# Optimization experiments

Measured on AMD Instinct MI355X. Metric: run time of the kernel, lower is better.

The kernel has to match this reference:

```python
import jax, jax.numpy as jnp
import numpy as np

NFIELD, NKER = 8, 16
B, Y, X, P, T = 32, 32, 32, 16, 8


def setup_inputs() -> dict:
    key = jax.random.key(0)
    k1, k2 = jax.random.split(key)
    fieldpatch = jax.random.normal(k1, (B, NFIELD, Y, X, P, T), dtype=jnp.float32)
    quadpatch = jax.random.uniform(k2, (B, Y, X, P, T), dtype=jnp.float32)
    zeros_fk = jnp.zeros((NFIELD, NKER), dtype=jnp.float32)
    return {
        "fieldpatch": fieldpatch,
        "quadpatch": quadpatch,
        "mean_lat": zeros_fk, "logstd_lat": zeros_fk,
        "mean_lon": zeros_fk, "logstd_lon": zeros_fk,
        "mean_lev": zeros_fk, "logstd_lev": zeros_fk,
        "logtau_time": zeros_fk,
    }


def _gaussian1d(mean, logstd, length):
    # (f, k, length): exp(-0.5*((coord - mean)/std)^2), coord in [-1, 1]
    coord = jnp.linspace(-1.0, 1.0, length, dtype=mean.dtype)
    std = jnp.exp(logstd)
    z = (coord[None, None, :] - mean[..., None]) / std[..., None]
    return jnp.exp(-0.5 * z * z)


def _exponential1d(logtau, length):
    # (f, k, length): exp(-coord / tau), coord = 0..length-1
    coord = jnp.arange(length, dtype=logtau.dtype)
    tau = jnp.exp(logtau) + 1e-4
    return jnp.exp(-coord[None, None, :] / tau[..., None])


def reference(fieldpatch, quadpatch, mean_lat, logstd_lat, mean_lon, logstd_lon,
              mean_lev, logstd_lev, logtau_time):
    b, f, y, x, p, t = fieldpatch.shape
    ky = _gaussian1d(mean_lat, logstd_lat, y)      # (f,k,y)
    kx = _gaussian1d(mean_lon, logstd_lon, x)      # (f,k,x)
    kp = _gaussian1d(mean_lev, logstd_lev, p)      # (f,k,p)
    kt = _exponential1d(logtau_time, t)            # (f,k,t)
    # Separable outer product -> full kernel (f,k,y,x,p,t)
    kernel = jnp.einsum('fky,fkx,fkp,fkt->fkyxpt', ky, kx, kp, kt)
    qmean = quadpatch.mean(axis=0)                 # (y,x,p,t)
    integral = jnp.einsum('fkyxpt,yxpt->fk', kernel, qmean) + 1e-4
    weights = kernel / integral[:, :, None, None, None, None]
    # torch weights() runs under @torch.no_grad(): weights are constant wrt autograd
    weights = jax.lax.stop_gradient(weights)
    features = jnp.einsum('bfyxpt,fkyxpt,byxpt->bfk', fieldpatch, weights, quadpatch)
    return features.reshape(b, -1)
```

## Files before the change

### kernel.cpp

```cpp
#include <hip/hip_runtime.h>
#include <math.h>

#define NF 8
#define NK 16
#define BB 32
#define YY 32
#define XX 32
#define PP 16
#define TT 8
#define YX (YY*XX)
#define PT (PP*TT)
#define YXPT (YX*PT)
#define CHUNKS 8
#define COLS_PER_BLOCK (YX/CHUNKS)
#define COLS_PER_WAVE  (COLS_PER_BLOCK/4)
#define MAIN_ITERS     (COLS_PER_WAVE/2)
#define STEP           ((2*PT)/4)

#define QMEAN_OFF 0
#define ACC_OFF   (QMEAN_OFF + YXPT)
#define INTG_OFF  (ACC_OFF + CHUNKS*BB*NF*NK)

__global__ __launch_bounds__(256) void k_qmean(const float* __restrict__ quad,
                                               float* __restrict__ ws) {
    const int tid = threadIdx.x, bx = blockIdx.x;
    __shared__ float4 sm[256];
    const int j4 = bx * 32 + (tid & 31);
    const int bg = tid >> 5;
    const float4* q4 = (const float4*)quad;
    float4 a = make_float4(0.f, 0.f, 0.f, 0.f);
    #pragma unroll
    for (int i = 0; i < 4; ++i) {
        float4 v = q4[(size_t)(bg * 4 + i) * (YXPT / 4) + j4];
        a.x += v.x; a.y += v.y; a.z += v.z; a.w += v.w;
    }
    sm[tid] = a;
    __syncthreads();
    if (tid < 32) {
        float4 r = sm[tid];
        #pragma unroll
        for (int g = 1; g < 8; ++g) {
            float4 v = sm[tid + 32 * g];
            r.x += v.x; r.y += v.y; r.z += v.z; r.w += v.w;
        }
        r.x *= (1.f / BB); r.y *= (1.f / BB); r.z *= (1.f / BB); r.w *= (1.f / BB);
        ((float4*)(ws + QMEAN_OFF))[j4] = r;
    }
}

__global__ __launch_bounds__(256) void k_integral(
    const float* __restrict__ mean_lat, const float* __restrict__ logstd_lat,
    const float* __restrict__ mean_lon, const float* __restrict__ logstd_lon,
    const float* __restrict__ mean_lev, const float* __restrict__ logstd_lev,
    const float* __restrict__ logtau, float* __restrict__ ws) {
    const int fk = blockIdx.x >> 2, qr = blockIdx.x & 3;
    const int tid = threadIdx.x;
    const float mlat = mean_lat[fk], islat = expf(-logstd_lat[fk]);
    const float mlon = mean_lon[fk], islon = expf(-logstd_lon[fk]);
    const float mlev = mean_lev[fk], islev = expf(-logstd_lev[fk]);
    const float itau = 1.f / (expf(logtau[fk]) + 1e-4f);

    __shared__ __align__(16) float wpt[PT];
    if (tid < PT) {
        const float cp = -1.f + 2.f * (float)(tid >> 3) / (PP - 1);
        const float zp = (cp - mlev) * islev;
        wpt[tid] = expf(-0.5f * zp * zp - (float)(tid & 7) * itau);
    }
    __syncthreads();

    const int yx = qr * 256 + tid;
    const float cy = -1.f + 2.f * (float)(yx >> 5) / (YY - 1);
    const float cx = -1.f + 2.f * (float)(yx & 31) / (XX - 1);
    const float zy = (cy - mlat) * islat;
    const float zx = (cx - mlon) * islon;
    const float wyx = expf(-0.5f * (zy * zy + zx * zx));

    const float4* q4 = (const float4*)(ws + QMEAN_OFF + (size_t)yx * PT);
    const float4* w4 = (const float4*)wpt;
    float s = 0.f;
    #pragma unroll
    for (int j = 0; j < PT / 4; ++j) {
        float4 w = w4[j], q = q4[j];
        s += w.x * q.x + w.y * q.y + w.z * q.z + w.w * q.w;
    }
    float partial = wyx * s;
    #pragma unroll
    for (int m = 32; m; m >>= 1) partial += __shfl_xor(partial, m);
    __shared__ float red[4];
    if ((tid & 63) == 0) red[tid >> 6] = partial;
    __syncthreads();
    if (tid == 0)
        ws[INTG_OFF + qr * (NF * NK) + fk] = red[0] + red[1] + red[2] + red[3];
}


#define KQ(WC, K) do {                                                          \
    float poly = fmaf(ga.w, r[K], ga.z);                                        \
    poly = fmaf(poly, r[K], ga.y);                                              \
    poly = fmaf(poly, r[K], ga.x);                                              \
    acc[K] = fmaf(WC, poly, acc[K]);                                            \
} while (0)

#define COLPAIR_COMPUTE(WVP) do {                                               \
    float4 ga;                                                                  \
    ga.x = fa.x*qa.x; ga.y = fa.y*qa.y; ga.z = fa.z*qa.z; ga.w = fa.w*qa.w;     \
    float4 w0 = (WVP)[0], w1 = (WVP)[1], w2 = (WVP)[2], w3 = (WVP)[3];          \
    KQ(w0.x, 0);  KQ(w0.y, 1);  KQ(w0.z, 2);  KQ(w0.w, 3);                      \
    KQ(w1.x, 4);  KQ(w1.y, 5);  KQ(w1.z, 6);  KQ(w1.w, 7);                      \
    KQ(w2.x, 8);  KQ(w2.y, 9);  KQ(w2.z, 10); KQ(w2.w, 11);                     \
    KQ(w3.x, 12); KQ(w3.y, 13); KQ(w3.z, 14); KQ(w3.w, 15);                     \
} while (0)

__global__ __launch_bounds__(256) void k_main(
    const float* __restrict__ field, const float* __restrict__ quad,
    const float* __restrict__ mean_lat, const float* __restrict__ logstd_lat,
    const float* __restrict__ mean_lon, const float* __restrict__ logstd_lon,
    const float* __restrict__ mean_lev, const float* __restrict__ logstd_lev,
    const float* __restrict__ logtau, float* __restrict__ ws)
{
    const int bx = blockIdx.x;
    const int qg2 = bx >> 6, f = (bx >> 3) & 7, rr0 = bx & 7;
    const int bc = qg2 * 8 + rr0;
    const int b = bc >> 3, chunk = bc & 7;
    const int tid = threadIdx.x;
    const int wave = tid >> 6, L = tid & 63;
    const int half = L >> 5, qg = L & 31;

    const int colBase = chunk * COLS_PER_BLOCK + wave * COLS_PER_WAVE;
    const float4* fp = (const float4*)(field + (size_t)(b * NF + f) * YXPT + (size_t)colBase * PT) + L;
    const float4* qp = (const float4*)(quad  + (size_t)b * YXPT            + (size_t)colBase * PT) + L;

    float4 fbuf[4], qbuf[4];
    #pragma unroll
    for (int j = 0; j < 4; ++j) { fbuf[j] = fp[j * STEP]; qbuf[j] = qp[j * STEP]; }

    __shared__ __align__(16) float sw[COLS_PER_BLOCK * NK];
    __shared__ float wptab[NK * PP];
    __shared__ float prm[NK][8];

    if (tid < NK) {
        const int fk = f * NK + tid;
        prm[tid][0] = mean_lat[fk];
        prm[tid][1] = expf(-logstd_lat[fk]);
        prm[tid][2] = mean_lon[fk];
        prm[tid][3] = expf(-logstd_lon[fk]);
        prm[tid][4] = mean_lev[fk];
        prm[tid][5] = expf(-logstd_lev[fk]);
        const float itau = 1.f / (expf(logtau[fk]) + 1e-4f);
        const float rk = expf(-itau);
        prm[tid][6] = rk;
        prm[tid][7] = rk * rk * rk * rk;
    }
    __syncthreads();

    #pragma unroll
    for (int i = 0; i < 8; ++i) {
        const int e = i * 256 + tid;
        const int col = e >> 4, k = e & 15;
        const int yx = chunk * COLS_PER_BLOCK + col;
        const float cy = -1.f + 2.f * (float)(yx >> 5) / (YY - 1);
        const float cx = -1.f + 2.f * (float)(yx & 31) / (XX - 1);
        const float zy = (cy - prm[k][0]) * prm[k][1];
        const float zx = (cx - prm[k][2]) * prm[k][3];
        sw[col * NK + k] = expf(-0.5f * (zy * zy + zx * zx));
    }
    {
        const int k = tid >> 4, p = tid & 15;
        const float cp = -1.f + 2.f * (float)p / (PP - 1);
        const float zp = (cp - prm[k][4]) * prm[k][5];
        wptab[tid] = expf(-0.5f * zp * zp);
    }
    __syncthreads();

    float r[NK];
    #pragma unroll
    for (int k = 0; k < NK; ++k)
        r[k] = __int_as_float(__builtin_amdgcn_readfirstlane(__float_as_int(prm[k][6])));

    float acc[NK];
    #pragma unroll
    for (int k = 0; k < NK; ++k) acc[k] = 0.f;

    const float* swp = sw + (wave * COLS_PER_WAVE + half) * NK;

    #pragma unroll 1
    for (int so = 0; so < 3; ++so) {
        fp += 4 * STEP; qp += 4 * STEP;
        #pragma unroll
        for (int j = 0; j < 4; ++j) {
            float4 fa = fbuf[j], qa = qbuf[j];
            fbuf[j] = fp[j * STEP]; qbuf[j] = qp[j * STEP];
            const float4* wvp = (const float4*)(swp + j * (2 * NK));
            COLPAIR_COMPUTE(wvp);
        }
        swp += 4 * (2 * NK);
    }
    #pragma unroll
    for (int j = 0; j < 4; ++j) {
        float4 fa = fbuf[j], qa = qbuf[j];
        const float4* wvp = (const float4*)(swp + j * (2 * NK));
        COLPAIR_COMPUTE(wvp);
    }

    {
        const int p = qg >> 1, hi = qg & 1;
        #pragma unroll
        for (int k = 0; k < NK; ++k) {
            const float wp = wptab[k * PP + p];
            const float ck = hi ? wp * prm[k][7] : wp;
            acc[k] *= ck;
        }
    }

    __shared__ float red[4][NK];
    #pragma unroll
    for (int k = 0; k < NK; ++k) {
        float v = acc[k];
        v += __shfl_xor(v, 32); v += __shfl_xor(v, 16); v += __shfl_xor(v, 8);
        v += __shfl_xor(v, 4);  v += __shfl_xor(v, 2);  v += __shfl_xor(v, 1);
        if (L == 0) red[wave][k] = v;
    }
    __syncthreads();
    if (tid < NK) {
        float s2 = red[0][tid] + red[1][tid] + red[2][tid] + red[3][tid];
        ws[ACC_OFF + chunk * (BB * NF * NK) + (b * NF + f) * NK + tid] = s2;
    }
}

__global__ void k_final(const float* __restrict__ ws, float* __restrict__ out) {
    int i = blockIdx.x * 256 + threadIdx.x;
    if (i >= BB * NF * NK) return;
    float a = 0.f;
    #pragma unroll
    for (int c = 0; c < CHUNKS; ++c) a += ws[ACC_OFF + c * (BB * NF * NK) + i];
    const int fk = i & (NF * NK - 1);
    float g = 1e-4f;
    #pragma unroll
    for (int q = 0; q < 4; ++q) g += ws[INTG_OFF + q * (NF * NK) + fk];
    out[i] = a / g;
}

extern "C" void kernel_launch(void* const* d_in, const int* in_sizes, int n_in,
                              void* d_out, int out_size, void* d_ws, size_t ws_size,
                              hipStream_t stream) {
    const float* field = (const float*)d_in[0];
    const float* quad  = (const float*)d_in[1];
    float* ws = (float*)d_ws;

    k_qmean<<<1024, 256, 0, stream>>>(quad, ws);
    k_integral<<<NF * NK * 4, 256, 0, stream>>>(
        (const float*)d_in[2], (const float*)d_in[3],
        (const float*)d_in[4], (const float*)d_in[5],
        (const float*)d_in[6], (const float*)d_in[7],
        (const float*)d_in[8], ws);
    k_main<<<BB * NF * CHUNKS, 256, 0, stream>>>(field, quad,
        (const float*)d_in[2], (const float*)d_in[3],
        (const float*)d_in[4], (const float*)d_in[5],
        (const float*)d_in[6], (const float*)d_in[7],
        (const float*)d_in[8], ws);
    k_final<<<(BB * NF * NK + 255) / 256, 256, 0, stream>>>(ws, (float*)d_out);
}
```

Baseline: 232.4 us.

## Merge qmean and main kernels into one launch, deepen prefetch to eight column pairs

The qmean reduction and the main feature-accumulation kernel become one launch. The first 1024 blocks compute the batch mean of quadpatch and the remaining blocks do the main work, so the two can run concurrently and one launch boundary is removed. The integral kernel moves after the fused kernel, which it needs since it reads the qmean. The main loop now prefetches all eight column pairs of a half at once instead of four per iteration, which raises memory-level parallelism at the cost of more registers.

```diff
diff --git a/kernel.cpp b/kernel.cpp
--- a/kernel.cpp
+++ b/kernel.cpp
@@ -14,84 +14,12 @@
 #define CHUNKS 8
 #define COLS_PER_BLOCK (YX/CHUNKS)
 #define COLS_PER_WAVE  (COLS_PER_BLOCK/4)
-#define MAIN_ITERS     (COLS_PER_WAVE/2)
 #define STEP           ((2*PT)/4)
+#define QMEAN_BLOCKS   1024
 
 #define QMEAN_OFF 0
 #define ACC_OFF   (QMEAN_OFF + YXPT)
 #define INTG_OFF  (ACC_OFF + CHUNKS*BB*NF*NK)
-
-__global__ __launch_bounds__(256) void k_qmean(const float* __restrict__ quad,
-                                               float* __restrict__ ws) {
-    const int tid = threadIdx.x, bx = blockIdx.x;
-    __shared__ float4 sm[256];
-    const int j4 = bx * 32 + (tid & 31);
-    const int bg = tid >> 5;
-    const float4* q4 = (const float4*)quad;
-    float4 a = make_float4(0.f, 0.f, 0.f, 0.f);
-    #pragma unroll
-    for (int i = 0; i < 4; ++i) {
-        float4 v = q4[(size_t)(bg * 4 + i) * (YXPT / 4) + j4];
-        a.x += v.x; a.y += v.y; a.z += v.z; a.w += v.w;
-    }
-    sm[tid] = a;
-    __syncthreads();
-    if (tid < 32) {
-        float4 r = sm[tid];
-        #pragma unroll
-        for (int g = 1; g < 8; ++g) {
-            float4 v = sm[tid + 32 * g];
-            r.x += v.x; r.y += v.y; r.z += v.z; r.w += v.w;
-        }
-        r.x *= (1.f / BB); r.y *= (1.f / BB); r.z *= (1.f / BB); r.w *= (1.f / BB);
-        ((float4*)(ws + QMEAN_OFF))[j4] = r;
-    }
-}
-
-__global__ __launch_bounds__(256) void k_integral(
-    const float* __restrict__ mean_lat, const float* __restrict__ logstd_lat,
-    const float* __restrict__ mean_lon, const float* __restrict__ logstd_lon,
-    const float* __restrict__ mean_lev, const float* __restrict__ logstd_lev,
-    const float* __restrict__ logtau, float* __restrict__ ws) {
-    const int fk = blockIdx.x >> 2, qr = blockIdx.x & 3;
-    const int tid = threadIdx.x;
-    const float mlat = mean_lat[fk], islat = expf(-logstd_lat[fk]);
-    const float mlon = mean_lon[fk], islon = expf(-logstd_lon[fk]);
-    const float mlev = mean_lev[fk], islev = expf(-logstd_lev[fk]);
-    const float itau = 1.f / (expf(logtau[fk]) + 1e-4f);
-
-    __shared__ __align__(16) float wpt[PT];
-    if (tid < PT) {
-        const float cp = -1.f + 2.f * (float)(tid >> 3) / (PP - 1);
-        const float zp = (cp - mlev) * islev;
-        wpt[tid] = expf(-0.5f * zp * zp - (float)(tid & 7) * itau);
-    }
-    __syncthreads();
-
-    const int yx = qr * 256 + tid;
-    const float cy = -1.f + 2.f * (float)(yx >> 5) / (YY - 1);
-    const float cx = -1.f + 2.f * (float)(yx & 31) / (XX - 1);
-    const float zy = (cy - mlat) * islat;
-    const float zx = (cx - mlon) * islon;
-    const float wyx = expf(-0.5f * (zy * zy + zx * zx));
-
-    const float4* q4 = (const float4*)(ws + QMEAN_OFF + (size_t)yx * PT);
-    const float4* w4 = (const float4*)wpt;
-    float s = 0.f;
-    #pragma unroll
-    for (int j = 0; j < PT / 4; ++j) {
-        float4 w = w4[j], q = q4[j];
-        s += w.x * q.x + w.y * q.y + w.z * q.z + w.w * q.w;
-    }
-    float partial = wyx * s;
-    #pragma unroll
-    for (int m = 32; m; m >>= 1) partial += __shfl_xor(partial, m);
-    __shared__ float red[4];
-    if ((tid & 63) == 0) red[tid >> 6] = partial;
-    __syncthreads();
-    if (tid == 0)
-        ws[INTG_OFF + qr * (NF * NK) + fk] = red[0] + red[1] + red[2] + red[3];
-}
 
 
 #define KQ(WC, K) do {                                                          \
@@ -111,18 +39,49 @@
     KQ(w3.x, 12); KQ(w3.y, 13); KQ(w3.z, 14); KQ(w3.w, 15);                     \
 } while (0)
 
-__global__ __launch_bounds__(256) void k_main(
+__global__ __launch_bounds__(256) void k_fused(
     const float* __restrict__ field, const float* __restrict__ quad,
     const float* __restrict__ mean_lat, const float* __restrict__ logstd_lat,
     const float* __restrict__ mean_lon, const float* __restrict__ logstd_lon,
     const float* __restrict__ mean_lev, const float* __restrict__ logstd_lev,
     const float* __restrict__ logtau, float* __restrict__ ws)
 {
-    const int bx = blockIdx.x;
+    const int tid = threadIdx.x;
+    const int bx0 = blockIdx.x;
+    __shared__ __align__(16) float smem[2432];
+    __shared__ float red[4][NK];
+
+    if (bx0 < QMEAN_BLOCKS) {
+        float4* sm = (float4*)smem;
+        const int j4 = bx0 * 32 + (tid & 31);
+        const int bg = tid >> 5;
+        const float4* q4 = (const float4*)quad;
+        float4 a = make_float4(0.f, 0.f, 0.f, 0.f);
+        #pragma unroll
+        for (int i = 0; i < 4; ++i) {
+            float4 v = q4[(size_t)(bg * 4 + i) * (YXPT / 4) + j4];
+            a.x += v.x; a.y += v.y; a.z += v.z; a.w += v.w;
+        }
+        sm[tid] = a;
+        __syncthreads();
+        if (tid < 32) {
+            float4 rr = sm[tid];
+            #pragma unroll
+            for (int g = 1; g < 8; ++g) {
+                float4 v = sm[tid + 32 * g];
+                rr.x += v.x; rr.y += v.y; rr.z += v.z; rr.w += v.w;
+            }
+            rr.x *= (1.f / BB); rr.y *= (1.f / BB);
+            rr.z *= (1.f / BB); rr.w *= (1.f / BB);
+            ((float4*)(ws + QMEAN_OFF))[j4] = rr;
+        }
+        return;
+    }
+
+    const int bx = bx0 - QMEAN_BLOCKS;
     const int qg2 = bx >> 6, f = (bx >> 3) & 7, rr0 = bx & 7;
     const int bc = qg2 * 8 + rr0;
     const int b = bc >> 3, chunk = bc & 7;
-    const int tid = threadIdx.x;
     const int wave = tid >> 6, L = tid & 63;
     const int half = L >> 5, qg = L & 31;
 
@@ -130,13 +89,13 @@
     const float4* fp = (const float4*)(field + (size_t)(b * NF + f) * YXPT + (size_t)colBase * PT) + L;
     const float4* qp = (const float4*)(quad  + (size_t)b * YXPT            + (size_t)colBase * PT) + L;
 
-    float4 fbuf[4], qbuf[4];
-    #pragma unroll
-    for (int j = 0; j < 4; ++j) { fbuf[j] = fp[j * STEP]; qbuf[j] = qp[j * STEP]; }
-
-    __shared__ __align__(16) float sw[COLS_PER_BLOCK * NK];
-    __shared__ float wptab[NK * PP];
-    __shared__ float prm[NK][8];
+    float4 fbuf[8], qbuf[8];
+    #pragma unroll
+    for (int j = 0; j < 8; ++j) { fbuf[j] = fp[j * STEP]; qbuf[j] = qp[j * STEP]; }
+
+    float* sw = smem;
+    float* wptab = smem + 2048;
+    float (*prm)[8] = (float (*)[8])(smem + 2304);
 
     if (tid < NK) {
         const int fk = f * NK + tid;
@@ -183,22 +142,21 @@
 
     const float* swp = sw + (wave * COLS_PER_WAVE + half) * NK;
 
-    #pragma unroll 1
-    for (int so = 0; so < 3; ++so) {
-        fp += 4 * STEP; qp += 4 * STEP;
+    {
+        const float4* fp2 = fp + 8 * STEP;
+        const float4* qp2 = qp + 8 * STEP;
         #pragma unroll
-        for (int j = 0; j < 4; ++j) {
+        for (int j = 0; j < 8; ++j) {
             float4 fa = fbuf[j], qa = qbuf[j];
-            fbuf[j] = fp[j * STEP]; qbuf[j] = qp[j * STEP];
+            fbuf[j] = fp2[j * STEP]; qbuf[j] = qp2[j * STEP];
             const float4* wvp = (const float4*)(swp + j * (2 * NK));
             COLPAIR_COMPUTE(wvp);
         }
-        swp += 4 * (2 * NK);
-    }
-    #pragma unroll
-    for (int j = 0; j < 4; ++j) {
+    }
+    #pragma unroll
+    for (int j = 0; j < 8; ++j) {
         float4 fa = fbuf[j], qa = qbuf[j];
-        const float4* wvp = (const float4*)(swp + j * (2 * NK));
+        const float4* wvp = (const float4*)(swp + (8 + j) * (2 * NK));
         COLPAIR_COMPUTE(wvp);
     }
 
@@ -212,7 +170,6 @@
         }
     }
 
-    __shared__ float red[4][NK];
     #pragma unroll
     for (int k = 0; k < NK; ++k) {
         float v = acc[k];
@@ -225,6 +182,51 @@
         float s2 = red[0][tid] + red[1][tid] + red[2][tid] + red[3][tid];
         ws[ACC_OFF + chunk * (BB * NF * NK) + (b * NF + f) * NK + tid] = s2;
     }
+}
+
+__global__ __launch_bounds__(256) void k_integral(
+    const float* __restrict__ mean_lat, const float* __restrict__ logstd_lat,
+    const float* __restrict__ mean_lon, const float* __restrict__ logstd_lon,
+    const float* __restrict__ mean_lev, const float* __restrict__ logstd_lev,
+    const float* __restrict__ logtau, float* __restrict__ ws) {
+    const int fk = blockIdx.x >> 2, qr = blockIdx.x & 3;
+    const int tid = threadIdx.x;
+    const float mlat = mean_lat[fk], islat = expf(-logstd_lat[fk]);
+    const float mlon = mean_lon[fk], islon = expf(-logstd_lon[fk]);
+    const float mlev = mean_lev[fk], islev = expf(-logstd_lev[fk]);
+    const float itau = 1.f / (expf(logtau[fk]) + 1e-4f);
+
+    __shared__ __align__(16) float wpt[PT];
+    if (tid < PT) {
+        const float cp = -1.f + 2.f * (float)(tid >> 3) / (PP - 1);
+        const float zp = (cp - mlev) * islev;
+        wpt[tid] = expf(-0.5f * zp * zp - (float)(tid & 7) * itau);
+    }
+    __syncthreads();
+
+    const int yx = qr * 256 + tid;
+    const float cy = -1.f + 2.f * (float)(yx >> 5) / (YY - 1);
+    const float cx = -1.f + 2.f * (float)(yx & 31) / (XX - 1);
+    const float zy = (cy - mlat) * islat;
+    const float zx = (cx - mlon) * islon;
+    const float wyx = expf(-0.5f * (zy * zy + zx * zx));
+
+    const float4* q4 = (const float4*)(ws + QMEAN_OFF + (size_t)yx * PT);
+    const float4* w4 = (const float4*)wpt;
+    float s = 0.f;
+    #pragma unroll
+    for (int j = 0; j < PT / 4; ++j) {
+        float4 w = w4[j], q = q4[j];
+        s += w.x * q.x + w.y * q.y + w.z * q.z + w.w * q.w;
+    }
+    float partial = wyx * s;
+    #pragma unroll
+    for (int m = 32; m; m >>= 1) partial += __shfl_xor(partial, m);
+    __shared__ float red[4];
+    if ((tid & 63) == 0) red[tid >> 6] = partial;
+    __syncthreads();
+    if (tid == 0)
+        ws[INTG_OFF + qr * (NF * NK) + fk] = red[0] + red[1] + red[2] + red[3];
 }
 
 __global__ void k_final(const float* __restrict__ ws, float* __restrict__ out) {
@@ -247,16 +249,15 @@
     const float* quad  = (const float*)d_in[1];
     float* ws = (float*)d_ws;
 
-    k_qmean<<<1024, 256, 0, stream>>>(quad, ws);
+    k_fused<<<QMEAN_BLOCKS + BB * NF * CHUNKS, 256, 0, stream>>>(field, quad,
+        (const float*)d_in[2], (const float*)d_in[3],
+        (const float*)d_in[4], (const float*)d_in[5],
+        (const float*)d_in[6], (const float*)d_in[7],
+        (const float*)d_in[8], ws);
     k_integral<<<NF * NK * 4, 256, 0, stream>>>(
         (const float*)d_in[2], (const float*)d_in[3],
         (const float*)d_in[4], (const float*)d_in[5],
         (const float*)d_in[6], (const float*)d_in[7],
         (const float*)d_in[8], ws);
-    k_main<<<BB * NF * CHUNKS, 256, 0, stream>>>(field, quad,
-        (const float*)d_in[2], (const float*)d_in[3],
-        (const float*)d_in[4], (const float*)d_in[5],
-        (const float*)d_in[6], (const float*)d_in[7],
-        (const float*)d_in[8], ws);
     k_final<<<(BB * NF * NK + 255) / 256, 256, 0, stream>>>(ws, (float*)d_out);
 }
```

Result: slower. 277.2 us (+19.2%).
